# Performance work log

Hardware: AMD Instinct MI355X
Metric: run time of the kernel (lower is better)

## Reference

```python
import jax, jax.numpy as jnp
import numpy as np

SCALE = 0.1  # literal .mul(0.1) in the source, not 1/sqrt(d_k)


def setup_inputs() -> dict:
    key = jax.random.key(0)
    kq, kk, kv = jax.random.split(key, 3)
    B, S, D, Dv = 8, 2048, 1024, 1024
    q = jax.random.normal(kq, (B, S, D), dtype=jnp.float32)
    k = jax.random.normal(kk, (B, D, S), dtype=jnp.float32)  # note [B, D, S]: matmul(q, k) with no transpose
    v = jax.random.normal(kv, (B, S, Dv), dtype=jnp.float32)
    return {"q": q, "k": k, "v": v}


def reference(q, k, v):
    # s = (q @ k) * 0.1 ; a = softmax(s, -1) ; dropout in eval -> identity ; r = a @ v
    s = jnp.einsum('bsd,bdt->bst', q, k) * SCALE  # [B, S, S]
    a = jax.nn.softmax(s, axis=-1)
    r = jnp.einsum('bst,btv->bsv', a, v)          # [B, S, Dv]
    return r
```

## Files before the change

kernel.cpp:

```cpp
#include <hip/hip_runtime.h>
#include <stdint.h>

#define SEQ 2048
#define DHK 1024
#define DHV 1024
#define NB 8

typedef __attribute__((ext_vector_type(8))) short bf16x8;
typedef __attribute__((ext_vector_type(4))) float f32x4;

__device__ __forceinline__ unsigned short f2bf(float f) {
    uint32_t u = __builtin_bit_cast(uint32_t, f);
    u += 0x7fffu + ((u >> 16) & 1u);
    return (unsigned short)(u >> 16);
}

__device__ __forceinline__ void gload_lds16(const unsigned short* g, unsigned short* l) {
    __builtin_amdgcn_global_load_lds(
        (const __attribute__((address_space(1))) void*)g,
        (__attribute__((address_space(3))) void*)l,
        16, 0, 0);
}

__global__ __launch_bounds__(256) void cvt_q(const float* __restrict__ in,
                                             unsigned short* __restrict__ out) {
    size_t i = ((size_t)blockIdx.x * 256 + threadIdx.x) * 16;
#pragma unroll
    for (int c = 0; c < 4; ++c) {
        float4 v = *(const float4*)(in + i + c * 4);
        ushort4 o;
        o.x = f2bf(v.x); o.y = f2bf(v.y); o.z = f2bf(v.z); o.w = f2bf(v.w);
        *(ushort4*)(out + i + c * 4) = o;
    }
}

__global__ __launch_bounds__(256) void tr_cvt(const float* __restrict__ in,
                                              unsigned short* __restrict__ out,
                                              int R, int C) {
    __shared__ float tile[64][65];
    int b  = blockIdx.z;
    int c0 = blockIdx.x * 64, r0 = blockIdx.y * 64;
    const float* ib = in + (size_t)b * R * C;
    unsigned short* ob = out + (size_t)b * R * C;
    int tr = threadIdx.x >> 4;
    int tc = (threadIdx.x & 15) * 4;
#pragma unroll
    for (int it = 0; it < 4; ++it) {
        int r = tr + it * 16;
        float4 v = *(const float4*)(ib + (size_t)(r0 + r) * C + c0 + tc);
        tile[r][tc + 0] = v.x; tile[r][tc + 1] = v.y;
        tile[r][tc + 2] = v.z; tile[r][tc + 3] = v.w;
    }
    __syncthreads();
#pragma unroll
    for (int it = 0; it < 4; ++it) {
        int c = tr + it * 16;
        ushort4 o;
        o.x = f2bf(tile[tc + 0][c]);
        o.y = f2bf(tile[tc + 1][c]);
        o.z = f2bf(tile[tc + 2][c]);
        o.w = f2bf(tile[tc + 3][c]);
        *(ushort4*)(ob + (size_t)(c0 + c) * R + r0 + tc) = o;
    }
}

template <int MODE>
__global__ __launch_bounds__(256) void attn_gemm(const unsigned short* __restrict__ A,
                                                 const unsigned short* __restrict__ Bt,
                                                 void* __restrict__ Cout,
                                                 float* __restrict__ L) {
    constexpr int K  = (MODE == 0) ? DHK : SEQ;
    constexpr int N  = (MODE == 0) ? SEQ : DHV;
    constexpr int GM = SEQ / 128;
    constexpr int PM = (MODE == 0) ? 8 : 4;
    constexpr int PN = (MODE == 0) ? 8 : 4;
    constexpr int NPM = GM / PM;

    __shared__ unsigned short As[2][128 * 64];
    __shared__ unsigned short Bs[2][128 * 64];

    int lid   = blockIdx.x;
    int batch = lid & 7;
    int t     = lid >> 3;
    int pi    = t / (PM * PN);
    int wio   = t % (PM * PN);
    int bm    = (pi % NPM) * PM + (wio % PM);
    int bn    = (pi / NPM) * PN + (wio / PM);

    const int tid  = threadIdx.x;
    const int wv   = tid >> 6;
    const int lane = tid & 63;
    const int wm   = wv & 1, wn = wv >> 1;
    const int m16  = lane & 15, q = lane >> 4;

    const unsigned short* Ab = A + (size_t)batch * SEQ * K;
    const unsigned short* Bb = Bt + (size_t)batch * N * K;

    const int lr8 = lane >> 3;
    const int g   = (lane & 7) ^ lr8;
    size_t gA[4], gB[4];
    int lofs[4];
#pragma unroll
    for (int c = 0; c < 4; ++c) {
        int rloc = wv * 32 + c * 8 + lr8;
        gA[c] = (size_t)(bm * 128 + rloc) * K + g * 8;
        gB[c] = (size_t)(bn * 128 + rloc) * K + g * 8;
        lofs[c] = (wv * 32 + c * 8) * 64;
    }

    f32x4 acc[4][4];
#pragma unroll
    for (int i = 0; i < 4; ++i)
#pragma unroll
        for (int j = 0; j < 4; ++j)
#pragma unroll
            for (int e = 0; e < 4; ++e) acc[i][j][e] = 0.0f;

    const int sw = m16 & 7;

#pragma unroll
    for (int c = 0; c < 4; ++c) gload_lds16(Ab + gA[c], &As[0][lofs[c]]);
#pragma unroll
    for (int c = 0; c < 4; ++c) gload_lds16(Bb + gB[c], &Bs[0][lofs[c]]);

    int p = 0;
    for (int kk = 0; kk < K; kk += 64) {
        __syncthreads();
        if (kk + 64 < K) {
            int np = p ^ 1;
#pragma unroll
            for (int c = 0; c < 4; ++c) gload_lds16(Ab + gA[c] + kk + 64, &As[np][lofs[c]]);
#pragma unroll
            for (int c = 0; c < 4; ++c) gload_lds16(Bb + gB[c] + kk + 64, &Bs[np][lofs[c]]);
        }
#pragma unroll
        for (int ss = 0; ss < 2; ++ss) {
            bf16x8 af[4], bfv[4];
#pragma unroll
            for (int tt = 0; tt < 4; ++tt) {
                int rl = wm * 64 + tt * 16 + m16;
                af[tt]  = *(const bf16x8*)&As[p][rl * 64 + ((ss * 4 + q) ^ sw) * 8];
                int rb = wn * 64 + tt * 16 + m16;
                bfv[tt] = *(const bf16x8*)&Bs[p][rb * 64 + ((ss * 4 + q) ^ sw) * 8];
            }
#pragma unroll
            for (int mt = 0; mt < 4; ++mt)
#pragma unroll
                for (int nt = 0; nt < 4; ++nt)
                    acc[mt][nt] = __builtin_amdgcn_mfma_f32_16x16x32_bf16(
                        af[mt], bfv[nt], acc[mt][nt], 0, 0, 0);
        }
        p ^= 1;
    }

    const int i0 = bm * 128 + wm * 64;
    const int t0 = bn * 128 + wn * 64;
    if (MODE == 0) {
        unsigned short* E = (unsigned short*)Cout + (size_t)batch * SEQ * N;
        float rs[4][4];
#pragma unroll
        for (int mt = 0; mt < 4; ++mt)
#pragma unroll
            for (int e = 0; e < 4; ++e) rs[mt][e] = 0.0f;
#pragma unroll
        for (int mt = 0; mt < 4; ++mt)
#pragma unroll
            for (int nt = 0; nt < 4; ++nt)
#pragma unroll
                for (int e = 0; e < 4; ++e) {
                    float v = __expf(0.1f * acc[mt][nt][e]);
                    int i = i0 + mt * 16 + q * 4 + e;
                    int tt = t0 + nt * 16 + m16;
                    E[(size_t)i * N + tt] = f2bf(v);
                    rs[mt][e] += v;
                }
#pragma unroll
        for (int mt = 0; mt < 4; ++mt)
#pragma unroll
            for (int e = 0; e < 4; ++e) {
                float v = rs[mt][e];
                v += __shfl_xor(v, 1);
                v += __shfl_xor(v, 2);
                v += __shfl_xor(v, 4);
                v += __shfl_xor(v, 8);
                if (m16 == 0) atomicAdd(&L[batch * SEQ + i0 + mt * 16 + q * 4 + e], v);
            }
    } else {
        float* O = (float*)Cout + (size_t)batch * SEQ * N;
#pragma unroll
        for (int mt = 0; mt < 4; ++mt)
#pragma unroll
            for (int e = 0; e < 4; ++e) {
                int i = i0 + mt * 16 + q * 4 + e;
                float inv = 1.0f / L[batch * SEQ + i];
#pragma unroll
                for (int nt = 0; nt < 4; ++nt) {
                    int tt = t0 + nt * 16 + m16;
                    O[(size_t)i * N + tt] = acc[mt][nt][e] * inv;
                }
            }
    }
}

extern "C" void kernel_launch(void* const* d_in, const int* in_sizes, int n_in,
                              void* d_out, int out_size, void* d_ws, size_t ws_size,
                              hipStream_t stream) {
    (void)in_sizes; (void)n_in; (void)out_size; (void)ws_size;
    const float* q = (const float*)d_in[0];
    const float* k = (const float*)d_in[1];
    const float* v = (const float*)d_in[2];

    char* ws = (char*)d_ws;
    unsigned short* Qb = (unsigned short*)(ws);
    unsigned short* Kt = (unsigned short*)(ws + 33554432);
    unsigned short* Vt = (unsigned short*)(ws + 67108864);
    unsigned short* E  = (unsigned short*)(ws + 100663296);
    float* L           = (float*)(ws + 167772160);

    hipMemsetAsync(L, 0, NB * SEQ * sizeof(float), stream);

    cvt_q<<<dim3((NB * SEQ * DHK) / (256 * 16)), dim3(256), 0, stream>>>(q, Qb);
    tr_cvt<<<dim3(SEQ / 64, DHK / 64, NB), dim3(256), 0, stream>>>(k, Kt, DHK, SEQ);
    tr_cvt<<<dim3(DHV / 64, SEQ / 64, NB), dim3(256), 0, stream>>>(v, Vt, SEQ, DHV);

    attn_gemm<0><<<dim3(NB * 16 * 16), dim3(256), 0, stream>>>(Qb, Kt, (void*)E, L);
    attn_gemm<1><<<dim3(NB * 16 * 8), dim3(256), 0, stream>>>(E, Vt, d_out, L);
}
```

Before: 390.7 us.

## Fuse conversion kernels and compute softmax row sums via ones-MFMA in second GEMM

Merges the Q conversion and the K/V transpose-convert kernels into one launch indexed by a flat block id. Removes the memset and the atomic row-sum reduction in the first GEMM. Instead, the second GEMM accumulates each row sum by multiplying the bf16 exp tile against a ones vector with extra MFMAs. This drops two launches, the memset and the atomics, at the cost of about 25% more MFMA work in the second GEMM. Row sums now come from the bf16-rounded values, which slightly changes the normalization.

```diff
diff --git a/kernel.cpp b/kernel.cpp
--- a/kernel.cpp
+++ b/kernel.cpp
@@ -22,24 +22,40 @@
         16, 0, 0);
 }
 
-__global__ __launch_bounds__(256) void cvt_q(const float* __restrict__ in,
-                                             unsigned short* __restrict__ out) {
-    size_t i = ((size_t)blockIdx.x * 256 + threadIdx.x) * 16;
-#pragma unroll
-    for (int c = 0; c < 4; ++c) {
-        float4 v = *(const float4*)(in + i + c * 4);
-        ushort4 o;
-        o.x = f2bf(v.x); o.y = f2bf(v.y); o.z = f2bf(v.z); o.w = f2bf(v.w);
-        *(ushort4*)(out + i + c * 4) = o;
-    }
-}
-
-__global__ __launch_bounds__(256) void tr_cvt(const float* __restrict__ in,
-                                              unsigned short* __restrict__ out,
-                                              int R, int C) {
+__global__ __launch_bounds__(256) void fused_cvt(const float* __restrict__ q,
+                                                 const float* __restrict__ k,
+                                                 const float* __restrict__ v,
+                                                 unsigned short* __restrict__ Qb,
+                                                 unsigned short* __restrict__ Kt,
+                                                 unsigned short* __restrict__ Vt) {
     __shared__ float tile[64][65];
-    int b  = blockIdx.z;
-    int c0 = blockIdx.x * 64, r0 = blockIdx.y * 64;
+    int bid = blockIdx.x;
+    if (bid < 4096) {
+        size_t i = ((size_t)bid * 256 + threadIdx.x) * 16;
+#pragma unroll
+        for (int c = 0; c < 4; ++c) {
+            float4 x = *(const float4*)(q + i + c * 4);
+            ushort4 o;
+            o.x = f2bf(x.x); o.y = f2bf(x.y); o.z = f2bf(x.z); o.w = f2bf(x.w);
+            *(ushort4*)(Qb + i + c * 4) = o;
+        }
+        return;
+    }
+    const float* in;
+    unsigned short* out;
+    int R, C, b, x, y;
+    if (bid < 8192) {
+        int id = bid - 4096;
+        b = id >> 9; int rem = id & 511;
+        x = rem & 31; y = rem >> 5;
+        in = k; out = Kt; R = DHK; C = SEQ;
+    } else {
+        int id = bid - 8192;
+        b = id >> 9; int rem = id & 511;
+        x = rem & 15; y = rem >> 4;
+        in = v; out = Vt; R = SEQ; C = DHV;
+    }
+    int c0 = x * 64, r0 = y * 64;
     const float* ib = in + (size_t)b * R * C;
     unsigned short* ob = out + (size_t)b * R * C;
     int tr = threadIdx.x >> 4;
@@ -47,9 +63,9 @@
 #pragma unroll
     for (int it = 0; it < 4; ++it) {
         int r = tr + it * 16;
-        float4 v = *(const float4*)(ib + (size_t)(r0 + r) * C + c0 + tc);
-        tile[r][tc + 0] = v.x; tile[r][tc + 1] = v.y;
-        tile[r][tc + 2] = v.z; tile[r][tc + 3] = v.w;
+        float4 w = *(const float4*)(ib + (size_t)(r0 + r) * C + c0 + tc);
+        tile[r][tc + 0] = w.x; tile[r][tc + 1] = w.y;
+        tile[r][tc + 2] = w.z; tile[r][tc + 3] = w.w;
     }
     __syncthreads();
 #pragma unroll
@@ -67,8 +83,7 @@
 template <int MODE>
 __global__ __launch_bounds__(256) void attn_gemm(const unsigned short* __restrict__ A,
                                                  const unsigned short* __restrict__ Bt,
-                                                 void* __restrict__ Cout,
-                                                 float* __restrict__ L) {
+                                                 void* __restrict__ Cout) {
     constexpr int K  = (MODE == 0) ? DHK : SEQ;
     constexpr int N  = (MODE == 0) ? SEQ : DHV;
     constexpr int GM = SEQ / 128;
@@ -116,6 +131,14 @@
 #pragma unroll
             for (int e = 0; e < 4; ++e) acc[i][j][e] = 0.0f;
 
+    f32x4 acc1[4];
+#pragma unroll
+    for (int i = 0; i < 4; ++i)
+#pragma unroll
+        for (int e = 0; e < 4; ++e) acc1[i][e] = 0.0f;
+    const short one_bf = (short)0x3F80;
+    const bf16x8 ones = {one_bf, one_bf, one_bf, one_bf, one_bf, one_bf, one_bf, one_bf};
+
     const int sw = m16 & 7;
 
 #pragma unroll
@@ -149,6 +172,12 @@
                 for (int nt = 0; nt < 4; ++nt)
                     acc[mt][nt] = __builtin_amdgcn_mfma_f32_16x16x32_bf16(
                         af[mt], bfv[nt], acc[mt][nt], 0, 0, 0);
+            if (MODE == 1) {
+#pragma unroll
+                for (int mt = 0; mt < 4; ++mt)
+                    acc1[mt] = __builtin_amdgcn_mfma_f32_16x16x32_bf16(
+                        af[mt], ones, acc1[mt], 0, 0, 0);
+            }
         }
         p ^= 1;
     }
@@ -157,33 +186,16 @@
     const int t0 = bn * 128 + wn * 64;
     if (MODE == 0) {
         unsigned short* E = (unsigned short*)Cout + (size_t)batch * SEQ * N;
-        float rs[4][4];
 #pragma unroll
         for (int mt = 0; mt < 4; ++mt)
 #pragma unroll
-            for (int e = 0; e < 4; ++e) rs[mt][e] = 0.0f;
-#pragma unroll
-        for (int mt = 0; mt < 4; ++mt)
-#pragma unroll
-            for (int nt = 0; nt < 4; ++nt)
-#pragma unroll
-                for (int e = 0; e < 4; ++e) {
-                    float v = __expf(0.1f * acc[mt][nt][e]);
-                    int i = i0 + mt * 16 + q * 4 + e;
+            for (int e = 0; e < 4; ++e) {
+                int i = i0 + mt * 16 + q * 4 + e;
+#pragma unroll
+                for (int nt = 0; nt < 4; ++nt) {
                     int tt = t0 + nt * 16 + m16;
-                    E[(size_t)i * N + tt] = f2bf(v);
-                    rs[mt][e] += v;
+                    E[(size_t)i * N + tt] = f2bf(__expf(0.1f * acc[mt][nt][e]));
                 }
-#pragma unroll
-        for (int mt = 0; mt < 4; ++mt)
-#pragma unroll
-            for (int e = 0; e < 4; ++e) {
-                float v = rs[mt][e];
-                v += __shfl_xor(v, 1);
-                v += __shfl_xor(v, 2);
-                v += __shfl_xor(v, 4);
-                v += __shfl_xor(v, 8);
-                if (m16 == 0) atomicAdd(&L[batch * SEQ + i0 + mt * 16 + q * 4 + e], v);
             }
     } else {
         float* O = (float*)Cout + (size_t)batch * SEQ * N;
@@ -192,7 +204,7 @@
 #pragma unroll
             for (int e = 0; e < 4; ++e) {
                 int i = i0 + mt * 16 + q * 4 + e;
-                float inv = 1.0f / L[batch * SEQ + i];
+                float inv = 1.0f / acc1[mt][e];
 #pragma unroll
                 for (int nt = 0; nt < 4; ++nt) {
                     int tt = t0 + nt * 16 + m16;
@@ -215,14 +227,8 @@
     unsigned short* Kt = (unsigned short*)(ws + 33554432);
     unsigned short* Vt = (unsigned short*)(ws + 67108864);
     unsigned short* E  = (unsigned short*)(ws + 100663296);
-    float* L           = (float*)(ws + 167772160);
-
-    hipMemsetAsync(L, 0, NB * SEQ * sizeof(float), stream);
-
-    cvt_q<<<dim3((NB * SEQ * DHK) / (256 * 16)), dim3(256), 0, stream>>>(q, Qb);
-    tr_cvt<<<dim3(SEQ / 64, DHK / 64, NB), dim3(256), 0, stream>>>(k, Kt, DHK, SEQ);
-    tr_cvt<<<dim3(DHV / 64, SEQ / 64, NB), dim3(256), 0, stream>>>(v, Vt, SEQ, DHV);
-
-    attn_gemm<0><<<dim3(NB * 16 * 16), dim3(256), 0, stream>>>(Qb, Kt, (void*)E, L);
-    attn_gemm<1><<<dim3(NB * 16 * 8), dim3(256), 0, stream>>>(E, Vt, d_out, L);
-}
+
+    fused_cvt<<<dim3(12288), dim3(256), 0, stream>>>(q, k, v, Qb, Kt, Vt);
+    attn_gemm<0><<<dim3(NB * 16 * 16), dim3(256), 0, stream>>>(Qb, Kt, (void*)E);
+    attn_gemm<1><<<dim3(NB * 16 * 8), dim3(256), 0, stream>>>(E, Vt, d_out);
+}
```

Measured after the change: 378.6 us. 3.1% less time.
